# Kernel tuning notes

Hardware: AMD Instinct MI355X
Metric: run time of the kernel (lower is better)

The kernel has to match this reference:

```python
import jax, jax.numpy as jnp
import numpy as np

GROUP_SIZES = (64, 128, 256, 96, 160, 224, 192, 288, 320, 112, 80, 48, 32, 16, 32)
LENGTH = 512
ALPHABET = 21


def setup_inputs() -> dict:
    key = jax.random.key(0)
    keys = jax.random.split(key, len(GROUP_SIZES) + 1)
    n_samples = int(sum(GROUP_SIZES))
    inp = {"x": jax.random.normal(keys[0], (n_samples, LENGTH, ALPHABET), dtype=jnp.float32)}
    for i, g in enumerate(GROUP_SIZES):
        inp[f"mat{i}"] = jax.random.normal(keys[i + 1], (g, g), dtype=jnp.float32)
    return inp


def reference(x, mat0, mat1, mat2, mat3, mat4, mat5, mat6, mat7, mat8, mat9,
              mat10, mat11, mat12, mat13, mat14):
    mats = (mat0, mat1, mat2, mat3, mat4, mat5, mat6, mat7, mat8, mat9,
            mat10, mat11, mat12, mat13, mat14)
    # Block-diagonal grouped matmul along the sample dim: out[sl] = mats_i @ x[sl].
    # Group boundaries are static Python ints, so slicing is jit-friendly.
    pieces = []
    start = 0
    for m, g in zip(mats, GROUP_SIZES):
        xg = x[start:start + g]  # (g, L, A)
        pieces.append(jnp.einsum('gh,hla->gla', m, xg))
        start += g
    return jnp.concatenate(pieces, axis=0)
```

## Files before the change

### kernel.cpp

```cpp
#include <hip/hip_runtime.h>
#include <hip/hip_bf16.h>

#define NCOL 10752
#define NROW 2048
#define NG 15
#define NTILES 23

typedef __bf16 bf16;
typedef __attribute__((ext_vector_type(8))) __bf16 bf16x8;
typedef __attribute__((ext_vector_type(4))) __bf16 bf16x4;
typedef __attribute__((ext_vector_type(4))) float f32x4;

__constant__ int c_gsize[NG]  = {64,128,256,96,160,224,192,288,320,112,80,48,32,16,32};
__constant__ int c_gstart[NG] = {0,64,192,448,544,704,928,1120,1408,1728,1840,1920,1968,2000,2016};
__constant__ int c_tgrp[NTILES] = {8,8,8,7,7,7,2,2,5,5,6,6,4,4,1,9,3,10,0,11,12,14,13};
__constant__ int c_trow[NTILES] = {0,128,256,0,128,256,0,128,0,128,0,128,0,128,0,0,0,0,0,0,0,0,0};

struct MatPtrs { const float* p[NG]; };

constexpr int BM = 128, BN = 128, BK = 32, BKp = 40;

__global__ __launch_bounds__(256)
void matapply_kernel(const float* __restrict__ x, MatPtrs mats, float* __restrict__ out)
{
    __shared__ bf16 sA[2][BM][BKp];
    __shared__ bf16 sB[2][BN][BKp];

    const int tid    = threadIdx.x;
    const int colb   = blockIdx.x * BN;
    const int tileid = blockIdx.y;

    const int grp  = c_tgrp[tileid];
    const int row0 = c_trow[tileid];
    const int g    = c_gsize[grp];
    const int s    = c_gstart[grp];
    const float* __restrict__ M = mats.p[grp];

    const int wave = tid >> 6;
    const int lane = tid & 63;
    const int wr   = (wave & 1) * 64;
    const int wc   = (wave >> 1) * 64;
    const int lm   = lane & 15;
    const int kq   = lane >> 4;
    const int kb   = kq * 8;

    const int aK = (tid & 7) * 4;
    const int aR = tid >> 3;
    const int bC = (tid & 31) * 4;
    const int bK = (tid >> 5) * 4;

    const int nIter = (g + BK - 1) / BK;

    f32x4 acc[4][4];
    #pragma unroll
    for (int i = 0; i < 4; i++)
        #pragma unroll
        for (int j = 0; j < 4; j++)
            acc[i][j] = (f32x4){0.f, 0.f, 0.f, 0.f};

    float4 av[4], xv[4];

    #pragma unroll
    for (int i = 0; i < 4; i++) {
        int r = aR + 32 * i;
        av[i] = make_float4(0.f, 0.f, 0.f, 0.f);
        if ((row0 + r) < g && aK < g)
            av[i] = *(const float4*)(M + (size_t)(row0 + r) * g + aK);
    }
    #pragma unroll
    for (int j = 0; j < 4; j++)
        xv[j] = *(const float4*)(x + (size_t)(s + bK + j) * NCOL + colb + bC);

    #pragma unroll
    for (int i = 0; i < 4; i++) {
        int r = aR + 32 * i;
        bf16x4 w;
        w[0] = (bf16)av[i].x; w[1] = (bf16)av[i].y; w[2] = (bf16)av[i].z; w[3] = (bf16)av[i].w;
        *(bf16x4*)&sA[0][r][aK] = w;
    }
    #pragma unroll
    for (int cc = 0; cc < 4; cc++) {
        int lc = bC + cc;
        bf16x4 w;
        #pragma unroll
        for (int j = 0; j < 4; j++)
            w[j] = (bf16)(((const float*)&xv[j])[cc]);
        *(bf16x4*)&sB[0][lc][bK ^ (((lc >> 2) & 3) << 3)] = w;
    }
    __syncthreads();

    for (int it = 0; it < nIter; ++it) {
        const int cur = it & 1;
        const bool more = (it + 1) < nIter;

        if (more) {
            const int k0 = (it + 1) * BK;
            #pragma unroll
            for (int i = 0; i < 4; i++) {
                int r = aR + 32 * i;
                av[i] = make_float4(0.f, 0.f, 0.f, 0.f);
                if ((row0 + r) < g && (k0 + aK) < g)
                    av[i] = *(const float4*)(M + (size_t)(row0 + r) * g + (k0 + aK));
            }
            #pragma unroll
            for (int j = 0; j < 4; j++)
                xv[j] = *(const float4*)(x + (size_t)(s + k0 + bK + j) * NCOL + colb + bC);
        }

        bf16x8 af[4], bfr[4];
        #pragma unroll
        for (int i = 0; i < 4; i++)
            af[i] = *(const bf16x8*)&sA[cur][wr + i * 16 + lm][kb];
        #pragma unroll
        for (int j = 0; j < 4; j++) {
            int lc = wc + j * 16 + lm;
            bfr[j] = *(const bf16x8*)&sB[cur][lc][kb ^ (((lc >> 2) & 3) << 3)];
        }
        #pragma unroll
        for (int i = 0; i < 4; i++)
            #pragma unroll
            for (int j = 0; j < 4; j++)
                acc[i][j] = __builtin_amdgcn_mfma_f32_16x16x32_bf16(af[i], bfr[j], acc[i][j], 0, 0, 0);

        if (more) {
            const int nxt = 1 - cur;
            #pragma unroll
            for (int i = 0; i < 4; i++) {
                int r = aR + 32 * i;
                bf16x4 w;
                w[0] = (bf16)av[i].x; w[1] = (bf16)av[i].y; w[2] = (bf16)av[i].z; w[3] = (bf16)av[i].w;
                *(bf16x4*)&sA[nxt][r][aK] = w;
            }
            #pragma unroll
            for (int cc = 0; cc < 4; cc++) {
                int lc = bC + cc;
                bf16x4 w;
                #pragma unroll
                for (int j = 0; j < 4; j++)
                    w[j] = (bf16)(((const float*)&xv[j])[cc]);
                *(bf16x4*)&sB[nxt][lc][bK ^ (((lc >> 2) & 3) << 3)] = w;
            }
            __syncthreads();
        }
    }

    #pragma unroll
    for (int i = 0; i < 4; i++) {
        #pragma unroll
        for (int r = 0; r < 4; r++) {
            int row = row0 + wr + i * 16 + kq * 4 + r;
            if (row < g) {
                float* orow = out + (size_t)(s + row) * NCOL + colb + wc;
                #pragma unroll
                for (int j = 0; j < 4; j++)
                    orow[j * 16 + lm] = acc[i][j][r];
            }
        }
    }
}

extern "C" void kernel_launch(void* const* d_in, const int* in_sizes, int n_in,
                              void* d_out, int out_size, void* d_ws, size_t ws_size,
                              hipStream_t stream)
{
    const float* x = (const float*)d_in[0];
    MatPtrs mp;
    for (int i = 0; i < NG; i++) mp.p[i] = (const float*)d_in[1 + i];
    float* out = (float*)d_out;

    dim3 grid(NCOL / BN, NTILES);
    dim3 block(256);
    matapply_kernel<<<grid, block, 0, stream>>>(x, mp, out);
}
```

Baseline: 192.8 us.

## Load A fragments directly from global into registers, skip A shared staging

Each lane now loads its own MFMA A-operand rows of the small group matrix straight from global memory into registers and converts them to bf16 there. This removes the sA shared buffer, its stores and its reads. The B shared-memory XOR swizzle key changes from (lc>>2) to (lc>>3), and launch bounds ask for 4 blocks per CU. The cost is redundant global loads of M across waves that share rows, which should mostly hit in cache, plus more register pressure from the prefetched float4 pairs.

```diff
diff --git a/kernel.cpp b/kernel.cpp
--- a/kernel.cpp
+++ b/kernel.cpp
@@ -20,10 +20,9 @@
 
 constexpr int BM = 128, BN = 128, BK = 32, BKp = 40;
 
-__global__ __launch_bounds__(256)
+__global__ __launch_bounds__(256, 4)
 void matapply_kernel(const float* __restrict__ x, MatPtrs mats, float* __restrict__ out)
 {
-    __shared__ bf16 sA[2][BM][BKp];
     __shared__ bf16 sB[2][BN][BKp];
 
     const int tid    = threadIdx.x;
@@ -44,8 +43,6 @@
     const int kq   = lane >> 4;
     const int kb   = kq * 8;
 
-    const int aK = (tid & 7) * 4;
-    const int aR = tid >> 3;
     const int bC = (tid & 31) * 4;
     const int bK = (tid >> 5) * 4;
 
@@ -58,26 +55,30 @@
         for (int j = 0; j < 4; j++)
             acc[i][j] = (f32x4){0.f, 0.f, 0.f, 0.f};
 
-    float4 av[4], xv[4];
+    float4 xv[4];
+    float4 a4[4][2];
+
+    int arow[4]; bool arok[4];
+    #pragma unroll
+    for (int i = 0; i < 4; i++) {
+        arow[i] = row0 + wr + i * 16 + lm;
+        arok[i] = arow[i] < g;
+    }
 
     #pragma unroll
     for (int i = 0; i < 4; i++) {
-        int r = aR + 32 * i;
-        av[i] = make_float4(0.f, 0.f, 0.f, 0.f);
-        if ((row0 + r) < g && aK < g)
-            av[i] = *(const float4*)(M + (size_t)(row0 + r) * g + aK);
+        a4[i][0] = make_float4(0.f,0.f,0.f,0.f);
+        a4[i][1] = make_float4(0.f,0.f,0.f,0.f);
+        if (arok[i] && kb < g) {
+            const float* p = M + (size_t)arow[i] * g + kb;
+            a4[i][0] = *(const float4*)p;
+            a4[i][1] = *(const float4*)(p + 4);
+        }
     }
     #pragma unroll
     for (int j = 0; j < 4; j++)
         xv[j] = *(const float4*)(x + (size_t)(s + bK + j) * NCOL + colb + bC);
 
-    #pragma unroll
-    for (int i = 0; i < 4; i++) {
-        int r = aR + 32 * i;
-        bf16x4 w;
-        w[0] = (bf16)av[i].x; w[1] = (bf16)av[i].y; w[2] = (bf16)av[i].z; w[3] = (bf16)av[i].w;
-        *(bf16x4*)&sA[0][r][aK] = w;
-    }
     #pragma unroll
     for (int cc = 0; cc < 4; cc++) {
         int lc = bC + cc;
@@ -85,7 +86,7 @@
         #pragma unroll
         for (int j = 0; j < 4; j++)
             w[j] = (bf16)(((const float*)&xv[j])[cc]);
-        *(bf16x4*)&sB[0][lc][bK ^ (((lc >> 2) & 3) << 3)] = w;
+        *(bf16x4*)&sB[0][lc][bK ^ (((lc >> 3) & 3) << 3)] = w;
     }
     __syncthreads();
 
@@ -93,28 +94,38 @@
         const int cur = it & 1;
         const bool more = (it + 1) < nIter;
 
+        bf16x8 af[4];
+        #pragma unroll
+        for (int i = 0; i < 4; i++) {
+            #pragma unroll
+            for (int e = 0; e < 4; e++) {
+                af[i][e]     = (bf16)(((const float*)&a4[i][0])[e]);
+                af[i][4 + e] = (bf16)(((const float*)&a4[i][1])[e]);
+            }
+        }
+
         if (more) {
             const int k0 = (it + 1) * BK;
             #pragma unroll
             for (int i = 0; i < 4; i++) {
-                int r = aR + 32 * i;
-                av[i] = make_float4(0.f, 0.f, 0.f, 0.f);
-                if ((row0 + r) < g && (k0 + aK) < g)
-                    av[i] = *(const float4*)(M + (size_t)(row0 + r) * g + (k0 + aK));
+                a4[i][0] = make_float4(0.f,0.f,0.f,0.f);
+                a4[i][1] = make_float4(0.f,0.f,0.f,0.f);
+                if (arok[i] && (k0 + kb) < g) {
+                    const float* p = M + (size_t)arow[i] * g + k0 + kb;
+                    a4[i][0] = *(const float4*)p;
+                    a4[i][1] = *(const float4*)(p + 4);
+                }
             }
             #pragma unroll
             for (int j = 0; j < 4; j++)
                 xv[j] = *(const float4*)(x + (size_t)(s + k0 + bK + j) * NCOL + colb + bC);
         }
 
-        bf16x8 af[4], bfr[4];
-        #pragma unroll
-        for (int i = 0; i < 4; i++)
-            af[i] = *(const bf16x8*)&sA[cur][wr + i * 16 + lm][kb];
+        bf16x8 bfr[4];
         #pragma unroll
         for (int j = 0; j < 4; j++) {
             int lc = wc + j * 16 + lm;
-            bfr[j] = *(const bf16x8*)&sB[cur][lc][kb ^ (((lc >> 2) & 3) << 3)];
+            bfr[j] = *(const bf16x8*)&sB[cur][lc][kb ^ (((lc >> 3) & 3) << 3)];
         }
         #pragma unroll
         for (int i = 0; i < 4; i++)
@@ -125,20 +136,13 @@
         if (more) {
             const int nxt = 1 - cur;
             #pragma unroll
-            for (int i = 0; i < 4; i++) {
-                int r = aR + 32 * i;
-                bf16x4 w;
-                w[0] = (bf16)av[i].x; w[1] = (bf16)av[i].y; w[2] = (bf16)av[i].z; w[3] = (bf16)av[i].w;
-                *(bf16x4*)&sA[nxt][r][aK] = w;
-            }
-            #pragma unroll
             for (int cc = 0; cc < 4; cc++) {
                 int lc = bC + cc;
                 bf16x4 w;
                 #pragma unroll
                 for (int j = 0; j < 4; j++)
                     w[j] = (bf16)(((const float*)&xv[j])[cc]);
-                *(bf16x4*)&sB[nxt][lc][bK ^ (((lc >> 2) & 3) << 3)] = w;
+                *(bf16x4*)&sB[nxt][lc][bK ^ (((lc >> 3) & 3) << 3)] = w;
             }
             __syncthreads();
         }
```

Result: slower. 381.1 us (+97.7%).
